# Kernel optimization log

Hardware: AMD Instinct MI355X
Metric: run time of the kernel (lower is better)

## Reference

```python
import jax, jax.numpy as jnp
import numpy as np

N_NODES, N_EDGES, N_GRAPHS = 50000, 800000, 512
F_IN, HID, DIM_OUT = 128, 256, 16


def setup_inputs() -> dict:
    key = jax.random.key(0)
    ks = jax.random.split(key, 16)
    glorot = lambda k, fi, fo: jax.random.normal(k, (fi, fo), jnp.float32) * jnp.sqrt(2.0 / (fi + fo))
    return {
        "x": jax.random.normal(ks[0], (N_NODES, F_IN), jnp.float32),
        "edge_index": jax.random.randint(ks[1], (2, N_EDGES), 0, N_NODES, dtype=jnp.int32),
        "batch": jnp.sort(jax.random.randint(ks[2], (N_NODES,), 0, N_GRAPHS, dtype=jnp.int32)),
        "mol_wt": jax.random.uniform(ks[3], (N_GRAPHS, 1), jnp.float32),
        "n_rings": jax.random.uniform(ks[4], (N_GRAPHS, 1), jnp.float32),
        "W1": glorot(ks[5], F_IN, HID), "b1": jnp.zeros((HID,), jnp.float32),
        "W2": glorot(ks[6], HID, HID), "b2": jnp.zeros((HID,), jnp.float32),
        "W3": glorot(ks[7], HID, HID), "b3": jnp.zeros((HID,), jnp.float32),
        "fcW1": glorot(ks[8], HID + 2, 196), "fcb1": jnp.zeros((196,), jnp.float32),
        "fcW2": glorot(ks[9], 196, DIM_OUT), "fcb2": jnp.zeros((DIM_OUT,), jnp.float32),
    }


def _gcn_conv(x, W, b, src, dst, deg_inv_sqrt, n_nodes):
    # PyG GCNConv: linear transform, then D^-1/2 (A+I) D^-1/2 aggregation, then bias
    xw = x @ W  # [N, HID]
    norm = deg_inv_sqrt[src] * deg_inv_sqrt[dst]  # [E+N]
    msg = norm[:, None] * xw[src]  # gather + scale
    out = jax.ops.segment_sum(msg, dst, num_segments=n_nodes)  # scatter-add at targets
    return out + b


def reference(x, edge_index, batch, mol_wt, n_rings,
              W1, b1, W2, b2, W3, b3, fcW1, fcb1, fcW2, fcb2):
    n_nodes = x.shape[0]
    self_loop = jnp.arange(n_nodes, dtype=edge_index.dtype)
    src = jnp.concatenate([edge_index[0], self_loop])
    dst = jnp.concatenate([edge_index[1], self_loop])
    deg = jax.ops.segment_sum(jnp.ones_like(dst, dtype=x.dtype), dst, num_segments=n_nodes)
    deg_inv_sqrt = jnp.where(deg > 0, jax.lax.rsqrt(deg), 0.0)

    h = jax.nn.relu(_gcn_conv(x, W1, b1, src, dst, deg_inv_sqrt, n_nodes))
    h = jax.nn.relu(_gcn_conv(h, W2, b2, src, dst, deg_inv_sqrt, n_nodes))
    h = jax.nn.relu(_gcn_conv(h, W3, b3, src, dst, deg_inv_sqrt, n_nodes))

    n_graphs = mol_wt.shape[0]
    sums = jax.ops.segment_sum(h, batch, num_segments=n_graphs)
    counts = jax.ops.segment_sum(jnp.ones((n_nodes,), h.dtype), batch, num_segments=n_graphs)
    hg = sums / jnp.maximum(counts, 1.0)[:, None]  # global mean pool

    hg = jnp.concatenate([hg, mol_wt, n_rings], axis=1)  # [G, 258]
    hg = jax.nn.relu(hg @ fcW1 + fcb1)
    return hg @ fcW2 + fcb2
```

## Files before the change

### kernel.cpp

```cpp
#include <hip/hip_runtime.h>

#define NN 50000
#define NE 800000
#define NG 512
#define FIN 128
#define HID 256
#define NBUK 196

typedef short short8 __attribute__((ext_vector_type(8)));
typedef float f32x4 __attribute__((ext_vector_type(4)));
typedef unsigned short u16x8 __attribute__((ext_vector_type(8)));

static inline int cdiv(int a, int b) { return (a + b - 1) / b; }

static __device__ inline unsigned short f2bf(float f) {
    unsigned int u = __float_as_uint(f);
    unsigned int r = (u + 0x7FFF + ((u >> 16) & 1)) >> 16;
    return (unsigned short)r;
}
static __device__ inline float bf2f(unsigned short h) {
    return __uint_as_float(((unsigned int)h) << 16);
}
static __device__ inline float bflo(unsigned int p) { return __uint_as_float(p << 16); }
static __device__ inline float bfhi(unsigned int p) { return __uint_as_float(p & 0xFFFF0000u); }

typedef __attribute__((address_space(1))) unsigned int gu32;
typedef __attribute__((address_space(3))) unsigned int lu32;
static __device__ __forceinline__ void gload16(const unsigned short* g, unsigned short* l) {
    __builtin_amdgcn_global_load_lds((const gu32*)(const void*)g, (lu32*)(void*)l, 16, 0, 0);
}


__global__ __launch_bounds__(256) void hist_bucket_kernel(const int* __restrict__ dst,
                                                          int* __restrict__ gbuk) {
    __shared__ int lh[NBUK];
    int tid = threadIdx.x;
    for (int j = tid; j < NBUK; j += 256) lh[j] = 0;
    __syncthreads();
    int base = blockIdx.x * 2048;
    #pragma unroll
    for (int k = 0; k < 8; ++k) {
        int i = base + k * 256 + tid;
        if (i < NE) atomicAdd(&lh[dst[i] >> 8], 1);
    }
    __syncthreads();
    for (int j = tid; j < NBUK; j += 256) if (lh[j]) atomicAdd(&gbuk[j], lh[j]);
}

__global__ void goff_kernel(const int* __restrict__ batch, int* __restrict__ goff) {
    int i = blockIdx.x * 256 + threadIdx.x;
    if (i >= NN) return;
    int b = batch[i];
    int pb = (i == 0) ? -1 : batch[i - 1];
    for (int g = pb + 1; g <= b; ++g) goff[g] = i;
    if (i == NN - 1) for (int g = b + 1; g <= NG; ++g) goff[g] = NN;
}

__global__ void buk_scan_kernel(const int* __restrict__ gbuk, int* __restrict__ bukoff,
                                int* __restrict__ bukcur) {
    __shared__ int ws[4];
    int tid = threadIdx.x, lane = tid & 63, wid = tid >> 6;
    int v = (tid < NBUK) ? gbuk[tid] : 0;
    int incl = v;
    #pragma unroll
    for (int off = 1; off < 64; off <<= 1) {
        int u = __shfl_up(incl, off, 64);
        if (lane >= off) incl += u;
    }
    if (lane == 63) ws[wid] = incl;
    __syncthreads();
    int woff = 0;
    for (int w = 0; w < wid; ++w) woff += ws[w];
    int ex = woff + incl - v;
    if (tid < NBUK) { bukoff[tid] = ex; bukcur[tid] = ex; }
    if (tid == NBUK - 1) bukoff[NBUK] = ex + v;
}

__global__ __launch_bounds__(256) void scatter_kernel(const int* __restrict__ src,
                                                      const int* __restrict__ dst,
                                                      int* __restrict__ bukcur,
                                                      unsigned int* __restrict__ pairs) {
    __shared__ int lh[NBUK];
    __shared__ int lbase[NBUK];
    int tid = threadIdx.x;
    for (int j = tid; j < NBUK; j += 256) lh[j] = 0;
    __syncthreads();
    int base = blockIdx.x * 2048;
    int d[8], s[8];
    #pragma unroll
    for (int k = 0; k < 8; ++k) {
        int i = base + k * 256 + tid;
        if (i < NE) {
            d[k] = dst[i]; s[k] = src[i];
            atomicAdd(&lh[d[k] >> 8], 1);
        } else d[k] = -1;
    }
    __syncthreads();
    for (int j = tid; j < NBUK; j += 256) lbase[j] = lh[j] ? atomicAdd(&bukcur[j], lh[j]) : 0;
    __syncthreads();
    for (int j = tid; j < NBUK; j += 256) lh[j] = 0;
    __syncthreads();
    #pragma unroll
    for (int k = 0; k < 8; ++k) {
        if (d[k] >= 0) {
            int b = d[k] >> 8;
            int loc = atomicAdd(&lh[b], 1);
            pairs[lbase[b] + loc] = ((unsigned int)s[k] << 16) | (unsigned int)(d[k] & 255);
        }
    }
}

__global__ __launch_bounds__(256) void local_csr_kernel(const unsigned int* __restrict__ pairs,
                                                        const int* __restrict__ bukoff,
                                                        int* __restrict__ row_ptr,
                                                        int* __restrict__ col,
                                                        float* __restrict__ dis) {
    __shared__ int fcnt[256];
    __shared__ int foff[256];
    __shared__ int fws[4];
    int b = blockIdx.x, tid = threadIdx.x;
    int beg = bukoff[b], end = bukoff[b + 1];
    fcnt[tid] = 0;
    __syncthreads();
    for (int i = beg + tid; i < end; i += 256) atomicAdd(&fcnt[pairs[i] & 255], 1);
    __syncthreads();
    int lane = tid & 63, wid = tid >> 6;
    int v = fcnt[tid], incl = v;
    #pragma unroll
    for (int off = 1; off < 64; off <<= 1) {
        int u = __shfl_up(incl, off, 64);
        if (lane >= off) incl += u;
    }
    if (lane == 63) fws[wid] = incl;
    __syncthreads();
    int woff = 0;
    for (int w = 0; w < wid; ++w) woff += fws[w];
    int ex = woff + incl - v;
    foff[tid] = ex;
    int gid = b * 256 + tid;
    if (gid < NN) {
        row_ptr[gid] = beg + ex;
        dis[gid] = rsqrtf((float)v + 1.0f);
    }
    if (b == 0 && tid == 0) row_ptr[NN] = NE;
    __syncthreads();
    for (int i = beg + tid; i < end; i += 256) {
        unsigned int p = pairs[i];
        int loc = atomicAdd(&foff[p & 255], 1);
        col[beg + loc] = (int)(p >> 16);
    }
}

__global__ void cast_scale_kernel(const float* __restrict__ x, const float* __restrict__ dis,
                                  unsigned short* __restrict__ Xs, int n4) {
    int i = blockIdx.x * 256 + threadIdx.x;
    if (i < n4) {
        float dv = dis[i >> 5];
        float4 v = ((const float4*)x)[i];
        ushort4 o;
        o.x = f2bf(dv * v.x); o.y = f2bf(dv * v.y); o.z = f2bf(dv * v.z); o.w = f2bf(dv * v.w);
        ((ushort4*)Xs)[i] = o;
    }
}

__global__ void tcast_all_kernel(const float* __restrict__ W1, const float* __restrict__ W2,
                                 const float* __restrict__ W3,
                                 unsigned short* __restrict__ W1t, unsigned short* __restrict__ W2t,
                                 unsigned short* __restrict__ W3t) {
    int idx = blockIdx.x * 256 + threadIdx.x;
    if (idx < FIN * 256) {
        int n = idx / FIN, k = idx - n * FIN;
        W1t[idx] = f2bf(W1[(size_t)k * 256 + n]);
    } else if (idx < FIN * 256 + HID * 256) {
        int t = idx - FIN * 256;
        int n = t / HID, k = t - n * HID;
        W2t[t] = f2bf(W2[(size_t)k * 256 + n]);
    } else {
        int t = idx - FIN * 256 - HID * 256;
        int n = t / HID, k = t - n * HID;
        W3t[t] = f2bf(W3[(size_t)k * 256 + n]);
    }
}

#define CLD 136
template <int MODE>
__global__ __launch_bounds__(256) void gemm128_kernel(
        const unsigned short* __restrict__ A, const unsigned short* __restrict__ Bt,
        const float* __restrict__ dis, const float* __restrict__ bias,
        unsigned short* __restrict__ Cout, int M, int K) {
    __shared__ unsigned short smem[128 * CLD];
    unsigned short* As = smem;
    unsigned short* Bs = smem + 4096;
    const int tid = threadIdx.x;
    const int bm = blockIdx.x * 128, bn = blockIdx.y * 128;
    const int wave = tid >> 6, lane = tid & 63;
    const int l16 = lane & 15, quad = lane >> 4;
    const int wm = (wave & 1) * 64, wn = (wave >> 1) * 64;

    int srow0 = tid >> 2, skc = (tid & 3) * 8;
    int srow1 = (256 + tid) >> 2;
    int ar0 = bm + srow0; if (ar0 > M - 1) ar0 = M - 1;
    int ar1 = bm + srow1; if (ar1 > M - 1) ar1 = M - 1;

    f32x4 acc[4][4];
    #pragma unroll
    for (int i = 0; i < 4; ++i)
        #pragma unroll
        for (int j = 0; j < 4; ++j) acc[i][j] = (f32x4){0.f, 0.f, 0.f, 0.f};

    for (int k0 = 0; k0 < K; k0 += 32) {
        gload16(A + (size_t)ar0 * K + k0 + skc, &As[(size_t)tid * 8]);
        gload16(A + (size_t)ar1 * K + k0 + skc, &As[(size_t)(256 + tid) * 8]);
        gload16(Bt + (size_t)(bn + srow0) * K + k0 + skc, &Bs[(size_t)tid * 8]);
        gload16(Bt + (size_t)(bn + srow1) * K + k0 + skc, &Bs[(size_t)(256 + tid) * 8]);
        __syncthreads();
        short8 af[4], bf[4];
        #pragma unroll
        for (int mt = 0; mt < 4; ++mt) af[mt] = *(const short8*)&As[(wm + mt * 16 + l16) * 32 + quad * 8];
        #pragma unroll
        for (int nt = 0; nt < 4; ++nt) bf[nt] = *(const short8*)&Bs[(wn + nt * 16 + l16) * 32 + quad * 8];
        #pragma unroll
        for (int mt = 0; mt < 4; ++mt)
            #pragma unroll
            for (int nt = 0; nt < 4; ++nt)
                acc[mt][nt] = __builtin_amdgcn_mfma_f32_16x16x32_bf16(af[mt], bf[nt], acc[mt][nt], 0, 0, 0);
        __syncthreads();
    }
    float bv[4];
    #pragma unroll
    for (int nt = 0; nt < 4; ++nt) bv[nt] = bias[bn + wn + nt * 16 + l16];
    #pragma unroll
    for (int mt = 0; mt < 4; ++mt) {
        #pragma unroll
        for (int r = 0; r < 4; ++r) {
            int lrow = wm + mt * 16 + quad * 4 + r;
            int grow = bm + lrow; if (grow > M - 1) grow = M - 1;
            float dv = (MODE == 0) ? dis[grow] : 1.0f;
            #pragma unroll
            for (int nt = 0; nt < 4; ++nt) {
                float v = fmaxf(acc[mt][nt][r] + bv[nt], 0.f);
                if (MODE == 0) v *= dv;
                smem[lrow * CLD + wn + nt * 16 + l16] = f2bf(v);
            }
        }
    }
    __syncthreads();
    for (int c = tid; c < 2048; c += 256) {
        int lrow = c >> 4, coff = (c & 15) << 3;
        int grow = bm + lrow;
        if (grow < M)
            *(u16x8*)(Cout + (size_t)grow * HID + bn + coff) = *(const u16x8*)&smem[lrow * CLD + coff];
    }
}
#undef CLD

__global__ __launch_bounds__(256) void agg128_kernel(
        const unsigned short* __restrict__ Xs, const int* __restrict__ row_ptr,
        const int* __restrict__ col, const float* __restrict__ dis,
        unsigned short* __restrict__ Xa, int n) {
    int node = blockIdx.x * 4 + (threadIdx.x >> 6);
    if (node >= n) return;
    int lane = threadIdx.x & 63;
    const unsigned int* Xv = (const unsigned int*)Xs;
    unsigned int p = Xv[(size_t)node * 64 + lane];
    float ax = bflo(p), ay = bfhi(p);
    int e = row_ptr[node], end = row_ptr[node + 1];
    for (; e + 7 < end; e += 8) {
        unsigned int m[8];
        #pragma unroll
        for (int j = 0; j < 8; ++j) m[j] = Xv[(size_t)col[e + j] * 64 + lane];
        #pragma unroll
        for (int j = 0; j < 8; ++j) { ax += bflo(m[j]); ay += bfhi(m[j]); }
    }
    for (; e < end; ++e) {
        unsigned int m = Xv[(size_t)col[e] * 64 + lane];
        ax += bflo(m); ay += bfhi(m);
    }
    float dv = dis[node];
    unsigned int o = (unsigned int)f2bf(dv * ax) | ((unsigned int)f2bf(dv * ay) << 16);
    ((unsigned int*)Xa)[(size_t)node * 64 + lane] = o;
}

__global__ __launch_bounds__(256) void agg256_kernel(
        const unsigned short* __restrict__ Hs, const int* __restrict__ row_ptr,
        const int* __restrict__ col, const float* __restrict__ dis,
        unsigned short* __restrict__ G, int n) {
    int node = blockIdx.x * 4 + (threadIdx.x >> 6);
    if (node >= n) return;
    int lane = threadIdx.x & 63;
    const uint2* Hv = (const uint2*)Hs;
    uint2 p = Hv[(size_t)node * 64 + lane];
    float4 acc = make_float4(bflo(p.x), bfhi(p.x), bflo(p.y), bfhi(p.y));
    int e = row_ptr[node], end = row_ptr[node + 1];
    for (; e + 7 < end; e += 8) {
        uint2 m[8];
        #pragma unroll
        for (int j = 0; j < 8; ++j) m[j] = Hv[(size_t)col[e + j] * 64 + lane];
        #pragma unroll
        for (int j = 0; j < 8; ++j) {
            acc.x += bflo(m[j].x); acc.y += bfhi(m[j].x);
            acc.z += bflo(m[j].y); acc.w += bfhi(m[j].y);
        }
    }
    for (; e < end; ++e) {
        uint2 m = Hv[(size_t)col[e] * 64 + lane];
        acc.x += bflo(m.x); acc.y += bfhi(m.x);
        acc.z += bflo(m.y); acc.w += bfhi(m.y);
    }
    float dv = dis[node];
    ushort4 o;
    o.x = f2bf(dv * acc.x); o.y = f2bf(dv * acc.y);
    o.z = f2bf(dv * acc.z); o.w = f2bf(dv * acc.w);
    ((ushort4*)G)[(size_t)node * 64 + lane] = o;
}

__global__ __launch_bounds__(256) void pool_mlp_kernel(
        const unsigned short* __restrict__ H, const int* __restrict__ goff,
        const float* __restrict__ mol, const float* __restrict__ rings,
        const float* __restrict__ fcW1, const float* __restrict__ fcb1,
        const float* __restrict__ fcW2, const float* __restrict__ fcb2,
        float* __restrict__ out) {
    __shared__ float s_hg[258];
    __shared__ float s_t[196];
    int g = blockIdx.x, tid = threadIdx.x;
    int beg = goff[g], end = goff[g + 1];
    float acc = 0.f;
    for (int i = beg; i < end; ++i) acc += bf2f(H[(size_t)i * HID + tid]);
    s_hg[tid] = acc / fmaxf((float)(end - beg), 1.0f);
    if (tid == 0) { s_hg[256] = mol[g]; s_hg[257] = rings[g]; }
    __syncthreads();
    if (tid < 196) {
        float a = fcb1[tid];
        for (int k = 0; k < 258; ++k) a = fmaf(s_hg[k], fcW1[k * 196 + tid], a);
        s_t[tid] = fmaxf(a, 0.f);
    }
    __syncthreads();
    if (tid < 16) {
        float a = fcb2[tid];
        for (int k = 0; k < 196; ++k) a = fmaf(s_t[k], fcW2[k * 16 + tid], a);
        out[g * 16 + tid] = a;
    }
}

extern "C" void kernel_launch(void* const* d_in, const int* in_sizes, int n_in,
                              void* d_out, int out_size, void* d_ws, size_t ws_size,
                              hipStream_t stream) {
    const float* x     = (const float*)d_in[0];
    const int*   ei    = (const int*)d_in[1];
    const int*   batch = (const int*)d_in[2];
    const float* mol   = (const float*)d_in[3];
    const float* rings = (const float*)d_in[4];
    const float* W1 = (const float*)d_in[5];
    const float* b1 = (const float*)d_in[6];
    const float* W2 = (const float*)d_in[7];
    const float* b2 = (const float*)d_in[8];
    const float* W3 = (const float*)d_in[9];
    const float* b3 = (const float*)d_in[10];
    const float* fcW1 = (const float*)d_in[11];
    const float* fcb1 = (const float*)d_in[12];
    const float* fcW2 = (const float*)d_in[13];
    const float* fcb2 = (const float*)d_in[14];
    float* out = (float*)d_out;
    const int* src = ei;
    const int* dst = ei + NE;

    char* w = (char*)d_ws;
    auto alloc = [&](size_t bytes) {
        char* p = w;
        w += (bytes + 255) & ~(size_t)255;
        return p;
    };
    int*   gbuk    = (int*)alloc((size_t)NBUK * 4);
    int*   bukoff  = (int*)alloc((size_t)(NBUK + 1) * 4);
    int*   bukcur  = (int*)alloc((size_t)NBUK * 4);
    int*   row_ptr = (int*)alloc((size_t)(NN + 1) * 4);
    int*   goff    = (int*)alloc((size_t)(NG + 1) * 4);
    float* dis     = (float*)alloc((size_t)NN * 4);
    unsigned int* pairs = (unsigned int*)alloc((size_t)NE * 4);
    int*   col     = (int*)alloc((size_t)NE * 4);
    unsigned short* Xs  = (unsigned short*)alloc((size_t)NN * FIN * 2);
    unsigned short* Xa  = (unsigned short*)alloc((size_t)NN * FIN * 2);
    unsigned short* Hs  = (unsigned short*)alloc((size_t)NN * HID * 2);
    unsigned short* Ga  = (unsigned short*)alloc((size_t)NN * HID * 2);
    unsigned short* Hf  = (unsigned short*)alloc((size_t)NN * HID * 2);
    unsigned short* W1t = (unsigned short*)alloc((size_t)FIN * HID * 2);
    unsigned short* W2t = (unsigned short*)alloc((size_t)HID * HID * 2);
    unsigned short* W3t = (unsigned short*)alloc((size_t)HID * HID * 2);

    hipMemsetAsync(gbuk, 0, (size_t)NBUK * 4, stream);
    int eb = cdiv(NE, 2048);
    hist_bucket_kernel<<<eb, 256, 0, stream>>>(dst, gbuk);
    goff_kernel<<<cdiv(NN, 256), 256, 0, stream>>>(batch, goff);
    buk_scan_kernel<<<1, 256, 0, stream>>>(gbuk, bukoff, bukcur);
    scatter_kernel<<<eb, 256, 0, stream>>>(src, dst, bukcur, pairs);
    local_csr_kernel<<<NBUK, 256, 0, stream>>>(pairs, bukoff, row_ptr, col, dis);

    cast_scale_kernel<<<cdiv(NN * FIN / 4, 256), 256, 0, stream>>>(x, dis, Xs, NN * FIN / 4);
    tcast_all_kernel<<<cdiv((FIN + HID + HID) * 256, 256), 256, 0, stream>>>(W1, W2, W3, W1t, W2t, W3t);

    dim3 ggrid(cdiv(NN, 128), 2);
    int agrid = cdiv(NN, 4);
    agg128_kernel<<<agrid, 256, 0, stream>>>(Xs, row_ptr, col, dis, Xa, NN);
    gemm128_kernel<0><<<ggrid, 256, 0, stream>>>(Xa, W1t, dis, b1, Hs, NN, FIN);
    agg256_kernel<<<agrid, 256, 0, stream>>>(Hs, row_ptr, col, dis, Ga, NN);
    gemm128_kernel<0><<<ggrid, 256, 0, stream>>>(Ga, W2t, dis, b2, Hs, NN, HID);
    agg256_kernel<<<agrid, 256, 0, stream>>>(Hs, row_ptr, col, dis, Ga, NN);
    gemm128_kernel<1><<<ggrid, 256, 0, stream>>>(Ga, W3t, dis, b3, Hf, NN, HID);
    pool_mlp_kernel<<<NG, 256, 0, stream>>>(Hf, goff, mol, rings, fcW1, fcb1, fcW2, fcb2, out);
}
```

Before: 404.0 us.

## Store node features in column-sliced layout for cache-local gather aggregation

Feature matrices produced by the cast and first two GEMMs are now written in a sliced layout, where each 32-column slice of all nodes is contiguous. The aggregation kernels process one slice per block with 16 lanes per node, so concurrently running blocks gather from a smaller working set (about 3.2 MB per slice) that can stay in cache. Results are written back row-major with nontemporal stores. The cost is shorter 64-byte gather segments per neighbour, each slice re-reading the CSR indices, and more blocks.

Result: slower. 423.7 us (+4.9%).

```diff
diff --git a/kernel.cpp b/kernel.cpp
--- a/kernel.cpp
+++ b/kernel.cpp
@@ -152,14 +152,18 @@
 }
 
 __global__ void cast_scale_kernel(const float* __restrict__ x, const float* __restrict__ dis,
-                                  unsigned short* __restrict__ Xs, int n4) {
+                                  unsigned short* __restrict__ Xb, int n4) {
     int i = blockIdx.x * 256 + threadIdx.x;
     if (i < n4) {
-        float dv = dis[i >> 5];
+        int node = i >> 5;
+        int f4 = i & 31;
+        int s = f4 >> 3;
+        int o = f4 & 7;
+        float dv = dis[node];
         float4 v = ((const float4*)x)[i];
-        ushort4 o;
-        o.x = f2bf(dv * v.x); o.y = f2bf(dv * v.y); o.z = f2bf(dv * v.z); o.w = f2bf(dv * v.w);
-        ((ushort4*)Xs)[i] = o;
+        ushort4 w;
+        w.x = f2bf(dv * v.x); w.y = f2bf(dv * v.y); w.z = f2bf(dv * v.z); w.w = f2bf(dv * v.w);
+        ((ushort4*)Xb)[((size_t)s * NN + (size_t)node) * 8 + o] = w;
     }
 }
 
@@ -248,70 +252,52 @@
     for (int c = tid; c < 2048; c += 256) {
         int lrow = c >> 4, coff = (c & 15) << 3;
         int grow = bm + lrow;
-        if (grow < M)
-            *(u16x8*)(Cout + (size_t)grow * HID + bn + coff) = *(const u16x8*)&smem[lrow * CLD + coff];
+        if (grow < M) {
+            if (MODE == 0) {
+                int gcol = bn + coff;
+                int s = gcol >> 5, o = gcol & 31;
+                *(u16x8*)(Cout + ((size_t)s * M + (size_t)grow) * 32 + o) =
+                    *(const u16x8*)&smem[lrow * CLD + coff];
+            } else {
+                *(u16x8*)(Cout + (size_t)grow * HID + bn + coff) =
+                    *(const u16x8*)&smem[lrow * CLD + coff];
+            }
+        }
     }
 }
 #undef CLD
 
-__global__ __launch_bounds__(256) void agg128_kernel(
-        const unsigned short* __restrict__ Xs, const int* __restrict__ row_ptr,
+template <int S>
+__global__ __launch_bounds__(256) void agg_slice_kernel(
+        const unsigned short* __restrict__ Hb, const int* __restrict__ row_ptr,
         const int* __restrict__ col, const float* __restrict__ dis,
-        unsigned short* __restrict__ Xa, int n) {
-    int node = blockIdx.x * 4 + (threadIdx.x >> 6);
+        unsigned short* __restrict__ Out, int n) {
+    constexpr int LOGS = (S == 8) ? 3 : 2;
+    int bid = blockIdx.x;
+    int s = bid & (S - 1);
+    int chunk = bid >> LOGS;
+    int tid = threadIdx.x;
+    int node = chunk * 16 + (tid >> 4);
     if (node >= n) return;
-    int lane = threadIdx.x & 63;
-    const unsigned int* Xv = (const unsigned int*)Xs;
-    unsigned int p = Xv[(size_t)node * 64 + lane];
+    int lane16 = tid & 15;
+    const unsigned int* Hv = (const unsigned int*)Hb + (size_t)s * NN * 16;
+    unsigned int p = Hv[(size_t)node * 16 + lane16];
     float ax = bflo(p), ay = bfhi(p);
     int e = row_ptr[node], end = row_ptr[node + 1];
     for (; e + 7 < end; e += 8) {
         unsigned int m[8];
         #pragma unroll
-        for (int j = 0; j < 8; ++j) m[j] = Xv[(size_t)col[e + j] * 64 + lane];
+        for (int j = 0; j < 8; ++j) m[j] = Hv[(size_t)col[e + j] * 16 + lane16];
         #pragma unroll
         for (int j = 0; j < 8; ++j) { ax += bflo(m[j]); ay += bfhi(m[j]); }
     }
     for (; e < end; ++e) {
-        unsigned int m = Xv[(size_t)col[e] * 64 + lane];
+        unsigned int m = Hv[(size_t)col[e] * 16 + lane16];
         ax += bflo(m); ay += bfhi(m);
     }
     float dv = dis[node];
     unsigned int o = (unsigned int)f2bf(dv * ax) | ((unsigned int)f2bf(dv * ay) << 16);
-    ((unsigned int*)Xa)[(size_t)node * 64 + lane] = o;
-}
-
-__global__ __launch_bounds__(256) void agg256_kernel(
-        const unsigned short* __restrict__ Hs, const int* __restrict__ row_ptr,
-        const int* __restrict__ col, const float* __restrict__ dis,
-        unsigned short* __restrict__ G, int n) {
-    int node = blockIdx.x * 4 + (threadIdx.x >> 6);
-    if (node >= n) return;
-    int lane = threadIdx.x & 63;
-    const uint2* Hv = (const uint2*)Hs;
-    uint2 p = Hv[(size_t)node * 64 + lane];
-    float4 acc = make_float4(bflo(p.x), bfhi(p.x), bflo(p.y), bfhi(p.y));
-    int e = row_ptr[node], end = row_ptr[node + 1];
-    for (; e + 7 < end; e += 8) {
-        uint2 m[8];
-        #pragma unroll
-        for (int j = 0; j < 8; ++j) m[j] = Hv[(size_t)col[e + j] * 64 + lane];
-        #pragma unroll
-        for (int j = 0; j < 8; ++j) {
-            acc.x += bflo(m[j].x); acc.y += bfhi(m[j].x);
-            acc.z += bflo(m[j].y); acc.w += bfhi(m[j].y);
-        }
-    }
-    for (; e < end; ++e) {
-        uint2 m = Hv[(size_t)col[e] * 64 + lane];
-        acc.x += bflo(m.x); acc.y += bfhi(m.x);
-        acc.z += bflo(m.y); acc.w += bfhi(m.y);
-    }
-    float dv = dis[node];
-    ushort4 o;
-    o.x = f2bf(dv * acc.x); o.y = f2bf(dv * acc.y);
-    o.z = f2bf(dv * acc.z); o.w = f2bf(dv * acc.w);
-    ((ushort4*)G)[(size_t)node * 64 + lane] = o;
+    __builtin_nontemporal_store(o, (unsigned int*)Out + (size_t)node * (S * 16) + s * 16 + lane16);
 }
 
 __global__ __launch_bounds__(256) void pool_mlp_kernel(
@@ -399,12 +385,12 @@
     tcast_all_kernel<<<cdiv((FIN + HID + HID) * 256, 256), 256, 0, stream>>>(W1, W2, W3, W1t, W2t, W3t);
 
     dim3 ggrid(cdiv(NN, 128), 2);
-    int agrid = cdiv(NN, 4);
-    agg128_kernel<<<agrid, 256, 0, stream>>>(Xs, row_ptr, col, dis, Xa, NN);
+    int achunks = cdiv(NN, 16);
+    agg_slice_kernel<4><<<4 * achunks, 256, 0, stream>>>(Xs, row_ptr, col, dis, Xa, NN);
     gemm128_kernel<0><<<ggrid, 256, 0, stream>>>(Xa, W1t, dis, b1, Hs, NN, FIN);
-    agg256_kernel<<<agrid, 256, 0, stream>>>(Hs, row_ptr, col, dis, Ga, NN);
+    agg_slice_kernel<8><<<8 * achunks, 256, 0, stream>>>(Hs, row_ptr, col, dis, Ga, NN);
     gemm128_kernel<0><<<ggrid, 256, 0, stream>>>(Ga, W2t, dis, b2, Hs, NN, HID);
-    agg256_kernel<<<agrid, 256, 0, stream>>>(Hs, row_ptr, col, dis, Ga, NN);
+    agg_slice_kernel<8><<<8 * achunks, 256, 0, stream>>>(Hs, row_ptr, col, dis, Ga, NN);
     gemm128_kernel<1><<<ggrid, 256, 0, stream>>>(Ga, W3t, dis, b3, Hf, NN, HID);
     pool_mlp_kernel<<<NG, 256, 0, stream>>>(Hf, goff, mol, rings, fcW1, fcb1, fcW2, fcb2, out);
 }
```
